# Performance work log

Measured on AMD Instinct MI355X. Metric: run time of the kernel, lower is better.

## Reference

```python
import jax, jax.numpy as jnp
import numpy as np

ISQRT2 = 0.7071067811865476  # orthonormal haar reconstruction scale
SCENE_BOUND = 1.5

def _ihaar(a, d, axis):
    # inverse 1D haar along negative `axis`: interleave even/odd reconstructed samples
    e = (a + d) * ISQRT2
    o = (a - d) * ISQRT2
    st = jnp.stack([e, o], axis=axis)  # new axis lands right after target axis
    shp = list(a.shape)
    shp[axis] = shp[axis] * 2
    return st.reshape(shp)

def _idwt3(approx, det7):
    # approx: (C,D,D,D); det7: (7,C,D,D,D) in ptwt subband order
    # keys 'aad','ada','add','daa','dad','dda','ddd' over axes (z,y,x)=(-3,-2,-1)
    S = {(0, 0, 0): approx}
    keys = [(0, 0, 1), (0, 1, 0), (0, 1, 1), (1, 0, 0), (1, 0, 1), (1, 1, 0), (1, 1, 1)]
    for k, b in zip(keys, range(7)):
        S[k] = det7[b]
    T = {(i, j): _ihaar(S[(i, j, 0)], S[(i, j, 1)], -1) for i in (0, 1) for j in (0, 1)}
    U = {i: _ihaar(T[(i, 0)], T[(i, 1)], -2) for i in (0, 1)}
    return _ihaar(U[0], U[1], -3)  # (C,2D,2D,2D)

def _trilinear(vol, xyz, bound):
    # vol: (C,R,R,R); xyz: (N,3) world coords; grid_sample convention:
    # xyz[:,0]->x (last axis), xyz[:,1]->y, xyz[:,2]->z; align_corners=True
    R = vol.shape[-1]
    g = jnp.clip((xyz / bound + 1.0) * 0.5 * (R - 1), 0.0, R - 1)
    x, y, z = g[:, 0], g[:, 1], g[:, 2]
    x0f, y0f, z0f = jnp.floor(x), jnp.floor(y), jnp.floor(z)
    fx, fy, fz = x - x0f, y - y0f, z - z0f
    x0 = x0f.astype(jnp.int32); y0 = y0f.astype(jnp.int32); z0 = z0f.astype(jnp.int32)
    x1 = jnp.minimum(x0 + 1, R - 1); y1 = jnp.minimum(y0 + 1, R - 1); z1 = jnp.minimum(z0 + 1, R - 1)
    def gat(zi, yi, xi):
        return vol[:, zi, yi, xi]  # (C,N)
    out = (gat(z0, y0, x0) * ((1 - fz) * (1 - fy) * (1 - fx))
         + gat(z0, y0, x1) * ((1 - fz) * (1 - fy) * fx)
         + gat(z0, y1, x0) * ((1 - fz) * fy * (1 - fx))
         + gat(z0, y1, x1) * ((1 - fz) * fy * fx)
         + gat(z1, y0, x0) * (fz * (1 - fy) * (1 - fx))
         + gat(z1, y0, x1) * (fz * (1 - fy) * fx)
         + gat(z1, y1, x0) * (fz * fy * (1 - fx))
         + gat(z1, y1, x1) * (fz * fy * fx))
    return out.T  # (N,C)

def setup_inputs() -> dict:
    key = jax.random.key(0)
    k0, k1, k2, k3, k4 = jax.random.split(key, 5)
    xyz = jax.random.uniform(k0, (1000000, 3), dtype=jnp.float32,
                             minval=-SCENE_BOUND, maxval=SCENE_BOUND)
    approx = jax.random.normal(k1, (1, 8, 32, 32, 32), dtype=jnp.float32) * 0.01
    detail0 = jax.random.normal(k2, (7, 8, 32, 32, 32), dtype=jnp.float32) * 0.001
    detail1 = jax.random.normal(k3, (7, 8, 64, 64, 64), dtype=jnp.float32) * 0.001
    detail2 = jax.random.normal(k4, (7, 8, 128, 128, 128), dtype=jnp.float32) * 0.001
    return {"xyz": xyz, "approx": approx, "detail0": detail0,
            "detail1": detail1, "detail2": detail2}

def reference(xyz, approx, detail0, detail1, detail2):
    # Hierarchical inverse 3D DWT: 32 -> 64 (dense) -> 128 (dense) -> 256 (fine,
    # fully-occupied tiles == dense reconstruction), then trilinear query.
    vol = approx[0]  # (C,32,32,32)
    for det in (detail0, detail1, detail2):
        vol = _idwt3(vol, det)
    return _trilinear(vol, xyz, SCENE_BOUND)  # (N,C)
```

## Files before the change

### kernel.cpp

```cpp
#include <hip/hip_runtime.h>

static constexpr float HS3 = 0.35355339059327373f;

__device__ __forceinline__ void ihaar8(const float s[8], float o[8]) {
    float ex[8];
#pragma unroll
    for (int m = 0; m < 8; m += 2) { ex[m] = s[m] + s[m + 1]; ex[m + 1] = s[m] - s[m + 1]; }
    float ey[8];
#pragma unroll
    for (int i = 0; i < 2; ++i)
#pragma unroll
        for (int px = 0; px < 2; ++px) {
            ey[i * 4 + 0 + px] = ex[i * 4 + 0 + px] + ex[i * 4 + 2 + px];
            ey[i * 4 + 2 + px] = ex[i * 4 + 0 + px] - ex[i * 4 + 2 + px];
        }
#pragma unroll
    for (int q = 0; q < 4; ++q) {
        o[q]     = (ey[q] + ey[4 + q]) * HS3;
        o[4 + q] = (ey[q] - ey[4 + q]) * HS3;
    }
}

__device__ __forceinline__ unsigned short f2bf(float f) {
    unsigned int u = __float_as_uint(f);
    unsigned int r = (u + 0x7FFFu + ((u >> 16) & 1u)) >> 16;
    return (unsigned short)r;
}

__global__ void idwt_pass(const float* __restrict__ A, const float* __restrict__ det,
                          float* __restrict__ out, int R) {
    int tid = blockIdx.x * blockDim.x + threadIdx.x;
    int R3 = R * R * R;
    if (tid >= 8 * R3) return;
    int c = tid / R3;
    int rem = tid - c * R3;
    int Z = rem / (R * R);
    int r2 = rem - Z * (R * R);
    int Y = r2 / R;
    int X = r2 - Y * R;

    float s[8];
    s[0] = A[tid];
    const float* dp = det + (size_t)c * R3 + rem;
    size_t bs = (size_t)8 * R3;
#pragma unroll
    for (int b = 0; b < 7; ++b) s[b + 1] = dp[(size_t)b * bs];

    float o[8];
    ihaar8(s, o);

    int Ro = 2 * R;
    float2* out2 = reinterpret_cast<float2*>(out);
#pragma unroll
    for (int pz = 0; pz < 2; ++pz)
#pragma unroll
        for (int py = 0; py < 2; ++py) {
            size_t idx = ((size_t)(c * Ro + 2 * Z + pz) * Ro + (2 * Y + py)) * R + X;
            out2[idx] = make_float2(o[pz * 4 + py * 2 + 0], o[pz * 4 + py * 2 + 1]);
        }
}

__global__ __launch_bounds__(512) void idwt_passC2(const float* __restrict__ A,
                                                   const float* __restrict__ det,
                                                   unsigned short* __restrict__ out) {
    const int R3 = 128 * 128 * 128;
    __shared__ float4 lds4[64][64];

    int T0 = blockIdx.x * 256;
    int t = threadIdx.x;
    int wave = t >> 6, lane = t & 63;

#pragma unroll
    for (int k = 0; k < 8; ++k) {
        int s = wave * 8 + k;
        const float* base = (s < 8) ? (A + (size_t)s * R3) : (det + (size_t)(s - 8) * R3);
        const float4* src = reinterpret_cast<const float4*>(base) + (T0 >> 2);
        lds4[s][lane] = src[lane];
    }
    __syncthreads();

    int cell = t & 255;
    int h = t >> 8;
    int cid = T0 + cell;
    int Z = cid >> 14;
    int r2 = cid & 16383;
    int Y = r2 >> 7;
    int X = r2 & 127;

    const float* ld = reinterpret_cast<const float*>(&lds4[0][0]);

    float ob[8][4];
#pragma unroll
    for (int cc = 0; cc < 4; ++cc) {
        int c = h * 4 + cc;
        float s8[8];
        s8[0] = ld[c * 256 + cell];
#pragma unroll
        for (int b = 0; b < 7; ++b) s8[b + 1] = ld[(8 + b * 8 + c) * 256 + cell];
        float o[8];
        ihaar8(s8, o);
#pragma unroll
        for (int p = 0; p < 8; ++p) ob[p][cc] = o[p];
    }

    uint2* out2 = reinterpret_cast<uint2*>(out);
#pragma unroll
    for (int pz = 0; pz < 2; ++pz)
#pragma unroll
        for (int py = 0; py < 2; ++py)
#pragma unroll
            for (int px = 0; px < 2; ++px) {
                int p = pz * 4 + py * 2 + px;
                size_t vox = (((size_t)(2 * Z + pz) * 256 + (2 * Y + py)) * 256 + (2 * X + px));
                uint2 v;
                v.x = (unsigned int)f2bf(ob[p][0]) | ((unsigned int)f2bf(ob[p][1]) << 16);
                v.y = (unsigned int)f2bf(ob[p][2]) | ((unsigned int)f2bf(ob[p][3]) << 16);
                out2[vox * 2 + h] = v;
            }
}

__device__ __forceinline__ float map_grid(float v) {
    float g = (v * (1.0f / 1.5f) + 1.0f) * (0.5f * 255.0f);
    return fminf(fmaxf(g, 0.0f), 255.0f);
}

__global__ void sample_kernel(const float* __restrict__ xyz, const unsigned short* __restrict__ vol,
                              float* __restrict__ out, int N) {
    int i = blockIdx.x * blockDim.x + threadIdx.x;
    if (i >= N) return;
    float gx = map_grid(xyz[3 * i + 0]);
    float gy = map_grid(xyz[3 * i + 1]);
    float gz = map_grid(xyz[3 * i + 2]);
    float x0f = floorf(gx), y0f = floorf(gy), z0f = floorf(gz);
    int x0 = (int)x0f, y0 = (int)y0f, z0 = (int)z0f;
    float fx = gx - x0f, fy = gy - y0f, fz = gz - z0f;
    int x1 = min(x0 + 1, 255), y1 = min(y0 + 1, 255), z1 = min(z0 + 1, 255);
    float wx0 = 1.0f - fx, wy0 = 1.0f - fy, wz0 = 1.0f - fz;

    float acc[8];
#pragma unroll
    for (int k = 0; k < 8; ++k) acc[k] = 0.0f;

    auto corner = [&](int z, int y, int x, float w) {
        const uint4* v4 = reinterpret_cast<const uint4*>(vol + ((((size_t)z * 256 + y) * 256 + x) << 3));
        uint4 a = *v4;
        acc[0] += w * __uint_as_float(a.x << 16);
        acc[1] += w * __uint_as_float(a.x & 0xFFFF0000u);
        acc[2] += w * __uint_as_float(a.y << 16);
        acc[3] += w * __uint_as_float(a.y & 0xFFFF0000u);
        acc[4] += w * __uint_as_float(a.z << 16);
        acc[5] += w * __uint_as_float(a.z & 0xFFFF0000u);
        acc[6] += w * __uint_as_float(a.w << 16);
        acc[7] += w * __uint_as_float(a.w & 0xFFFF0000u);
    };
    corner(z0, y0, x0, wz0 * wy0 * wx0);
    corner(z0, y0, x1, wz0 * wy0 * fx);
    corner(z0, y1, x0, wz0 * fy * wx0);
    corner(z0, y1, x1, wz0 * fy * fx);
    corner(z1, y0, x0, fz * wy0 * wx0);
    corner(z1, y0, x1, fz * wy0 * fx);
    corner(z1, y1, x0, fz * fy * wx0);
    corner(z1, y1, x1, fz * fy * fx);

    float4* o4 = reinterpret_cast<float4*>(out + (size_t)i * 8);
    o4[0] = make_float4(acc[0], acc[1], acc[2], acc[3]);
    o4[1] = make_float4(acc[4], acc[5], acc[6], acc[7]);
}

extern "C" void kernel_launch(void* const* d_in, const int* in_sizes, int n_in,
                              void* d_out, int out_size, void* d_ws, size_t ws_size,
                              hipStream_t stream) {
    const float* xyz     = (const float*)d_in[0];
    const float* approx  = (const float*)d_in[1];
    const float* detail0 = (const float*)d_in[2];
    const float* detail1 = (const float*)d_in[3];
    const float* detail2 = (const float*)d_in[4];
    float* out = (float*)d_out;
    int N = in_sizes[0] / 3;

    char* ws = (char*)d_ws;
    float* vol1 = (float*)ws;
    float* vol2 = (float*)(ws + (size_t)8 * 1024 * 1024);
    unsigned short* vol3 = (unsigned short*)(ws + (size_t)72 * 1024 * 1024);

    {
        int total = 8 * 32 * 32 * 32;
        idwt_pass<<<(total + 255) / 256, 256, 0, stream>>>(approx, detail0, vol1, 32);
    }
    {
        int total = 8 * 64 * 64 * 64;
        idwt_pass<<<(total + 255) / 256, 256, 0, stream>>>(vol1, detail1, vol2, 64);
    }
    {
        int blocks = (128 * 128 * 128) / 256;
        idwt_passC2<<<blocks, 512, 0, stream>>>(vol2, detail2, vol3);
    }
    sample_kernel<<<(N + 255) / 256, 256, 0, stream>>>(xyz, vol3, out, N);
}
```

Baseline: 286.8 us.

## Fuse three inverse DWT levels into one kernel recomputing coarse rows per block

Replaces the three separate IDWT passes with a single kernel in which each block loads the needed coarse-level rows of approx/detail0 and detail1, reconstructs them in shared memory, and then builds the finest level. This removes the intermediate 64^3 and 128^3 volumes written to and read back from global memory, and two kernel launches. It adds redundant recomputation and reloading of the coarse rows across blocks, and stages detail2 into LDS as bf16, which adds rounding before the final transform.

```diff
diff --git a/kernel.cpp b/kernel.cpp
--- a/kernel.cpp
+++ b/kernel.cpp
@@ -26,77 +26,110 @@
     unsigned int r = (u + 0x7FFFu + ((u >> 16) & 1u)) >> 16;
     return (unsigned short)r;
 }
-
-__global__ void idwt_pass(const float* __restrict__ A, const float* __restrict__ det,
-                          float* __restrict__ out, int R) {
-    int tid = blockIdx.x * blockDim.x + threadIdx.x;
-    int R3 = R * R * R;
-    if (tid >= 8 * R3) return;
-    int c = tid / R3;
-    int rem = tid - c * R3;
-    int Z = rem / (R * R);
-    int r2 = rem - Z * (R * R);
-    int Y = r2 / R;
-    int X = r2 - Y * R;
-
-    float s[8];
-    s[0] = A[tid];
-    const float* dp = det + (size_t)c * R3 + rem;
-    size_t bs = (size_t)8 * R3;
-#pragma unroll
-    for (int b = 0; b < 7; ++b) s[b + 1] = dp[(size_t)b * bs];
-
-    float o[8];
-    ihaar8(s, o);
-
-    int Ro = 2 * R;
-    float2* out2 = reinterpret_cast<float2*>(out);
-#pragma unroll
-    for (int pz = 0; pz < 2; ++pz)
-#pragma unroll
-        for (int py = 0; py < 2; ++py) {
-            size_t idx = ((size_t)(c * Ro + 2 * Z + pz) * Ro + (2 * Y + py)) * R + X;
-            out2[idx] = make_float2(o[pz * 4 + py * 2 + 0], o[pz * 4 + py * 2 + 1]);
-        }
-}
-
-__global__ __launch_bounds__(512) void idwt_passC2(const float* __restrict__ A,
-                                                   const float* __restrict__ det,
-                                                   unsigned short* __restrict__ out) {
-    const int R3 = 128 * 128 * 128;
-    __shared__ float4 lds4[64][64];
-
-    int T0 = blockIdx.x * 256;
+__device__ __forceinline__ float bf2f(unsigned short u) {
+    return __uint_as_float((unsigned int)u << 16);
+}
+
+__global__ __launch_bounds__(512) void idwt_fused(const float* __restrict__ approx,
+                                                  const float* __restrict__ det0,
+                                                  const float* __restrict__ det1,
+                                                  const float* __restrict__ det2,
+                                                  unsigned short* __restrict__ out) {
+    __shared__ __align__(16) unsigned short ld2[56 * 256];
+    __shared__ __align__(16) float ld1[56 * 64];
+    __shared__ __align__(16) float ld0[64 * 32];
+    __shared__ __align__(16) float v1[8 * 64];
+    __shared__ __align__(16) float v2[16 * 128];
+
+    const int R3_2 = 128 * 128 * 128;
+    const int R3_1 = 64 * 64 * 64;
+    const int R3_0 = 32 * 32 * 32;
+
+    int blk = blockIdx.x;
+    int Z = blk >> 6;
+    int k = blk & 63;
+    int T0 = Z * 16384 + k * 256;
     int t = threadIdx.x;
     int wave = t >> 6, lane = t & 63;
 
-#pragma unroll
-    for (int k = 0; k < 8; ++k) {
-        int s = wave * 8 + k;
-        const float* base = (s < 8) ? (A + (size_t)s * R3) : (det + (size_t)(s - 8) * R3);
-        const float4* src = reinterpret_cast<const float4*>(base) + (T0 >> 2);
-        lds4[s][lane] = src[lane];
+    if (wave < 7) {
+        uint2* ld2u2 = reinterpret_cast<uint2*>(ld2);
+#pragma unroll
+        for (int q = 0; q < 8; ++q) {
+            int s = wave * 8 + q;
+            float4 v = reinterpret_cast<const float4*>(det2 + (size_t)s * R3_2 + T0)[lane];
+            uint2 pkd;
+            pkd.x = (unsigned int)f2bf(v.x) | ((unsigned int)f2bf(v.y) << 16);
+            pkd.y = (unsigned int)f2bf(v.z) | ((unsigned int)f2bf(v.w) << 16);
+            ld2u2[s * 64 + lane] = pkd;
+        }
+    }
+    {
+        int cz = Z >> 1, cy = k;
+        size_t rowoff = (size_t)cz * 4096 + (size_t)cy * 64;
+        float4* d = reinterpret_cast<float4*>(ld1);
+        {
+            int s = t >> 4, f = t & 15;
+            d[t] = reinterpret_cast<const float4*>(det1 + (size_t)s * R3_1 + rowoff)[f];
+        }
+        if (t < 384) {
+            int idx = t + 512;
+            int s = idx >> 4, f = idx & 15;
+            d[idx] = reinterpret_cast<const float4*>(det1 + (size_t)s * R3_1 + rowoff)[f];
+        }
+    }
+    {
+        int z0 = Z >> 2, y0 = k >> 1;
+        int s = t >> 3, f = t & 7;
+        const float* base = (s < 8) ? (approx + (size_t)s * R3_0) : (det0 + (size_t)(s - 8) * R3_0);
+        reinterpret_cast<float4*>(ld0)[t] = reinterpret_cast<const float4*>(base + z0 * 1024 + y0 * 32)[f];
     }
     __syncthreads();
 
-    int cell = t & 255;
-    int h = t >> 8;
+    if (t < 256) {
+        int c = t >> 5, x0 = t & 31;
+        float s8[8];
+        s8[0] = ld0[c * 32 + x0];
+#pragma unroll
+        for (int bb = 0; bb < 7; ++bb) s8[bb + 1] = ld0[(8 + bb * 8 + c) * 32 + x0];
+        float o[8];
+        ihaar8(s8, o);
+        int pz0 = (Z >> 1) & 1, py0 = k & 1;
+        v1[c * 64 + 2 * x0 + 0] = o[pz0 * 4 + py0 * 2 + 0];
+        v1[c * 64 + 2 * x0 + 1] = o[pz0 * 4 + py0 * 2 + 1];
+    }
+    __syncthreads();
+
+    {
+        int c = t >> 6, x1 = t & 63;
+        float s8[8];
+        s8[0] = v1[c * 64 + x1];
+#pragma unroll
+        for (int bb = 0; bb < 7; ++bb) s8[bb + 1] = ld1[(bb * 8 + c) * 64 + x1];
+        float o[8];
+        ihaar8(s8, o);
+        int pz1 = Z & 1;
+#pragma unroll
+        for (int py = 0; py < 2; ++py)
+#pragma unroll
+            for (int px = 0; px < 2; ++px)
+                v2[(c * 2 + py) * 128 + 2 * x1 + px] = o[pz1 * 4 + py * 2 + px];
+    }
+    __syncthreads();
+
+    int cell = t >> 1, h = t & 1;
     int cid = T0 + cell;
-    int Z = cid >> 14;
-    int r2 = cid & 16383;
-    int Y = r2 >> 7;
-    int X = r2 & 127;
-
-    const float* ld = reinterpret_cast<const float*>(&lds4[0][0]);
+    int Y = (cid >> 7) & 127, X = cid & 127;
+    int yb = cell >> 7;
 
     float ob[8][4];
 #pragma unroll
     for (int cc = 0; cc < 4; ++cc) {
         int c = h * 4 + cc;
         float s8[8];
-        s8[0] = ld[c * 256 + cell];
-#pragma unroll
-        for (int b = 0; b < 7; ++b) s8[b + 1] = ld[(8 + b * 8 + c) * 256 + cell];
+        s8[0] = v2[(c * 2 + yb) * 128 + X];
+#pragma unroll
+        for (int bb = 0; bb < 7; ++bb) s8[bb + 1] = bf2f(ld2[(bb * 8 + c) * 256 + cell]);
         float o[8];
         ihaar8(s8, o);
 #pragma unroll
@@ -139,7 +172,7 @@
 
     float acc[8];
 #pragma unroll
-    for (int k = 0; k < 8; ++k) acc[k] = 0.0f;
+    for (int kk = 0; kk < 8; ++kk) acc[kk] = 0.0f;
 
     auto corner = [&](int z, int y, int x, float w) {
         const uint4* v4 = reinterpret_cast<const uint4*>(vol + ((((size_t)z * 256 + y) * 256 + x) << 3));
@@ -178,22 +211,8 @@
     float* out = (float*)d_out;
     int N = in_sizes[0] / 3;
 
-    char* ws = (char*)d_ws;
-    float* vol1 = (float*)ws;
-    float* vol2 = (float*)(ws + (size_t)8 * 1024 * 1024);
-    unsigned short* vol3 = (unsigned short*)(ws + (size_t)72 * 1024 * 1024);
-
-    {
-        int total = 8 * 32 * 32 * 32;
-        idwt_pass<<<(total + 255) / 256, 256, 0, stream>>>(approx, detail0, vol1, 32);
-    }
-    {
-        int total = 8 * 64 * 64 * 64;
-        idwt_pass<<<(total + 255) / 256, 256, 0, stream>>>(vol1, detail1, vol2, 64);
-    }
-    {
-        int blocks = (128 * 128 * 128) / 256;
-        idwt_passC2<<<blocks, 512, 0, stream>>>(vol2, detail2, vol3);
-    }
+    unsigned short* vol3 = (unsigned short*)d_ws;
+
+    idwt_fused<<<8192, 512, 0, stream>>>(approx, detail0, detail1, detail2, vol3);
     sample_kernel<<<(N + 255) / 256, 256, 0, stream>>>(xyz, vol3, out, N);
 }
```

Measured after the change: 263.9 us. -8.0%, faster.
